# Kernel tuning notes

Measured on AMD Instinct MI355X. Metric: run time of the kernel, lower is better.

The kernel has to match this reference:

```python
import jax, jax.numpy as jnp
import numpy as np

NS = 100000  # senders
NR = 100000  # receivers
E = 600000   # edges
D = 128      # sender_dim = receiver_dim = edge_dim
EPS = 1e-5


def _layer_norm(x, g, b):
    mu = jnp.mean(x, axis=-1, keepdims=True)
    var = jnp.mean(jnp.square(x - mu), axis=-1, keepdims=True)
    return (x - mu) * jax.lax.rsqrt(var + EPS) * g + b


def _gcast_mlp(x, W, b, gamma, beta):
    # Faithful to GCastMLP.forward: z = silu(linear(x)); z = LN(silu(z))
    z = jax.nn.silu(x @ W.T + b)
    return _layer_norm(jax.nn.silu(z), gamma, beta)


def setup_inputs() -> dict:
    key = jax.random.key(0)
    ks = jax.random.split(key, 12)
    s = 1.0 / np.sqrt(3 * D)
    inp = {
        "sender_x": jax.random.normal(ks[0], (NS, D), jnp.float32),
        "receiver_x": jax.random.normal(ks[1], (NR, D), jnp.float32),
        "edge_index": jax.random.randint(ks[2], (2, E), 0, NR, jnp.int32),
        "edge_attr": jax.random.normal(ks[3], (E, D), jnp.float32),
        # edge MLP: in = sender+receiver+edge = 3D, out = edge_dim
        "We": jax.random.uniform(ks[4], (D, 3 * D), jnp.float32, -s, s),
        "be": jnp.zeros((D,), jnp.float32),
        "ge": jnp.ones((D,), jnp.float32),
        "bbe": jnp.zeros((D,), jnp.float32),
        # node MLP: in = receiver+edge = 2D, out = receiver_dim
        "Wn": jax.random.uniform(ks[5], (D, 2 * D), jnp.float32, -1.0 / np.sqrt(2 * D), 1.0 / np.sqrt(2 * D)),
        "bn": jnp.zeros((D,), jnp.float32),
        "gn": jnp.ones((D,), jnp.float32),
        "bbn": jnp.zeros((D,), jnp.float32),
        # sender MLP: square D -> D
        "Ws": jax.random.uniform(ks[6], (D, D), jnp.float32, -1.0 / np.sqrt(D), 1.0 / np.sqrt(D)),
        "bs": jnp.zeros((D,), jnp.float32),
        "gs": jnp.ones((D,), jnp.float32),
        "bbs": jnp.zeros((D,), jnp.float32),
    }
    return inp


def reference(sender_x, receiver_x, edge_index, edge_attr,
              We, be, ge, bbe, Wn, bn, gn, bbn, Ws, bs, gs, bbs):
    src, dst = edge_index[0], edge_index[1]
    # Edge encoder: gather endpoints, concat, MLP -> new edge features [E, D]
    edge_in = jnp.concatenate([sender_x[src], receiver_x[dst], edge_attr], axis=-1)
    edge_attr_p = _gcast_mlp(edge_in, We, be, ge, bbe)
    # Node encoder: scatter-sum messages (= new edge features) to receivers
    edge_aggr = jax.ops.segment_sum(edge_attr_p, dst, num_segments=receiver_x.shape[0])
    mesh_x_p = _gcast_mlp(jnp.concatenate([receiver_x, edge_aggr], axis=-1), Wn, bn, gn, bbn)
    # Residual updates
    sender_out = sender_x + _gcast_mlp(sender_x, Ws, bs, gs, bbs)
    receiver_out = receiver_x + mesh_x_p
    edge_out = edge_attr + edge_attr_p
    return (sender_out, receiver_out, edge_out)
```

## Files before the change

kernel.cpp:

```cpp
#include <hip/hip_runtime.h>
#include <stdint.h>


typedef __bf16 bf16x8 __attribute__((ext_vector_type(8)));
typedef float  f32x4  __attribute__((ext_vector_type(4)));

union U16B { uint4 u; bf16x8 v; };
union BFPK { __bf16 h[2]; unsigned int u; };
union BF1  { __bf16 h; unsigned short s; };

__device__ __forceinline__ float silu_f(float x) {
  return x * __builtin_amdgcn_rcpf(1.0f + __expf(-x));
}
__device__ __forceinline__ float bfu2f(unsigned int lo16) {
  return __uint_as_float(lo16 << 16);
}
__device__ __forceinline__ bf16x8 cvt8(float4 a, float4 b) {
  bf16x8 r;
  r[0] = (__bf16)a.x; r[1] = (__bf16)a.y; r[2] = (__bf16)a.z; r[3] = (__bf16)a.w;
  r[4] = (__bf16)b.x; r[5] = (__bf16)b.y; r[6] = (__bf16)b.z; r[7] = (__bf16)b.w;
  return r;
}

__global__ void cvt_weights_kernel(const float* __restrict__ We,
                                   const float* __restrict__ Wn,
                                   const float* __restrict__ Ws,
                                   unsigned short* __restrict__ out) {
  int i = blockIdx.x * 256 + threadIdx.x;
  if (i >= 6 * 16384) return;
  int panel = i >> 14;
  int r = (i >> 7) & 127;
  int csw = i & 127;
  int c_or = ((csw * 2) ^ ((r & 7) << 4)) >> 1;
  float f;
  if (panel < 3)      f = We[r * 384 + panel * 128 + c_or];
  else if (panel < 5) f = Wn[r * 256 + (panel - 3) * 128 + c_or];
  else                f = Ws[r * 128 + c_or];
  BF1 c; c.h = (__bf16)f;
  out[i] = c.s;
}

__global__ void cvt_rows_kernel(const float* __restrict__ in,
                                unsigned short* __restrict__ out, int n8) {
  int i = blockIdx.x * 256 + threadIdx.x;
  if (i >= n8) return;
  float4 a = reinterpret_cast<const float4*>(in)[2 * i];
  float4 b = reinterpret_cast<const float4*>(in)[2 * i + 1];
  U16B r; r.v = cvt8(a, b);
  reinterpret_cast<uint4*>(out)[i] = r.u;
}

__global__ void hist_kernel(const int* __restrict__ dst, int* __restrict__ counts, int E) {
  int i = blockIdx.x * 256 + threadIdx.x;
  if (i < E) atomicAdd(&counts[dst[i]], 1);
}

__global__ void scan1_kernel(const int* __restrict__ counts, int* __restrict__ pre,
                             int* __restrict__ blockSums, int n) {
  __shared__ int sh[256];
  const int t = threadIdx.x;
  const int base = blockIdx.x * 1024 + t * 4;
  int c0 = (base + 0 < n) ? counts[base + 0] : 0;
  int c1 = (base + 1 < n) ? counts[base + 1] : 0;
  int c2 = (base + 2 < n) ? counts[base + 2] : 0;
  int c3 = (base + 3 < n) ? counts[base + 3] : 0;
  int tot = c0 + c1 + c2 + c3;
  sh[t] = tot;
  __syncthreads();
  #pragma unroll
  for (int off = 1; off < 256; off <<= 1) {
    int v = (t >= off) ? sh[t - off] : 0;
    __syncthreads();
    sh[t] += v;
    __syncthreads();
  }
  int excl = sh[t] - tot;
  if (base + 0 < n) pre[base + 0] = excl;
  if (base + 1 < n) pre[base + 1] = excl + c0;
  if (base + 2 < n) pre[base + 2] = excl + c0 + c1;
  if (base + 3 < n) pre[base + 3] = excl + c0 + c1 + c2;
  if (t == 255) blockSums[blockIdx.x] = sh[255];
}

__global__ void scan2_kernel(int* __restrict__ blockSums, int nb) {
  __shared__ int sh[512];
  const int t = threadIdx.x;
  int v = (t < nb) ? blockSums[t] : 0;
  sh[t] = v;
  __syncthreads();
  #pragma unroll
  for (int off = 1; off < 512; off <<= 1) {
    int u = (t >= off) ? sh[t - off] : 0;
    __syncthreads();
    sh[t] += u;
    __syncthreads();
  }
  if (t < nb) blockSums[t] = sh[t] - v;
}

__global__ void scan3_kernel(const int* __restrict__ pre, const int* __restrict__ blockSums,
                             int* __restrict__ offs, int* __restrict__ cursor, int n) {
  int i = blockIdx.x * 256 + threadIdx.x;
  if (i >= n) return;
  int o = pre[i] + blockSums[i >> 10];
  offs[i] = o;
  cursor[i] = o;
}

__global__ void scatter_kernel(const int* __restrict__ dst, int* __restrict__ cursor,
                               int* __restrict__ rank, int E) {
  int i = blockIdx.x * 256 + threadIdx.x;
  if (i < E) {
    int p = atomicAdd(&cursor[dst[i]], 1);
    rank[i] = p;
  }
}

__global__ __launch_bounds__(256) void agg_kernel(
    const unsigned short* __restrict__ P,
    const int* __restrict__ offs, const int* __restrict__ counts,
    unsigned short* __restrict__ aggr, int NR) {
  const int l = threadIdx.x & 31;
  const int g0 = (blockIdx.x * 256 + threadIdx.x) >> 5;
  if (g0 >= NR) return;
  int beg = offs[g0];
  int cnt = counts[g0];
  float s0 = 0.f, s1 = 0.f, s2 = 0.f, s3 = 0.f;
  const unsigned short* p = P + (size_t)beg * 128 + l * 4;
  for (int k = 0; k < cnt; ++k) {
    uint2 w = *reinterpret_cast<const uint2*>(p);
    p += 128;
    s0 += bfu2f(w.x & 0xffffu);
    s1 += bfu2f(w.x >> 16);
    s2 += bfu2f(w.y & 0xffffu);
    s3 += bfu2f(w.y >> 16);
  }
  BFPK a, b;
  a.h[0] = (__bf16)s0; a.h[1] = (__bf16)s1;
  b.h[0] = (__bf16)s2; b.h[1] = (__bf16)s3;
  uint2 o; o.x = a.u; o.y = b.u;
  *reinterpret_cast<uint2*>(aggr + (size_t)g0 * 128 + l * 4) = o;
}

template <int KDIM, int AGGR, bool S0B, bool S1B>
__global__ __launch_bounds__(512, 4) void mlp_v8_kernel(
    const void* __restrict__ s0v, const int* __restrict__ i0,
    const void* __restrict__ s1v, const int* __restrict__ i1,
    const float* __restrict__ s2,
    const unsigned short* __restrict__ Wb,
    const float* __restrict__ bias, const float* __restrict__ gamma,
    const float* __restrict__ beta,
    const float* __restrict__ resid,
    float* __restrict__ outp,
    void* aggr, const int* __restrict__ aggr_idx,
    const int* __restrict__ prank,
    int M) {
  constexpr int NSEG = KDIM / 128;
  __shared__ __align__(16) unsigned short smem[2][16384];

  const int tid = threadIdx.x;
  const int wid = tid >> 6;
  const int lane = tid & 63;
  const int l15 = lane & 15;
  const int q = lane >> 4;
  const int l31 = lane & 31;
  const int rhalf = lane >> 5;
  const int wrow = blockIdx.x * 128 + wid * 16;
  const int xm = (l15 & 7) << 3;

  int rr = wrow + l15;
  if (rr >= M) rr = M - 1;
  const unsigned short* p0b; const float* p0f;
  const unsigned short* p1b = nullptr; const float* p1f = nullptr;
  const float* p2 = nullptr;
  {
    int r0 = i0 ? i0[rr] : rr;
    if constexpr (S0B) p0b = (const unsigned short*)s0v + (size_t)r0 * 128;
    else               p0f = (const float*)s0v + (size_t)r0 * 128;
    if constexpr (KDIM >= 256) {
      int r1 = i1 ? i1[rr] : rr;
      if constexpr (S1B) p1b = (const unsigned short*)s1v + (size_t)r1 * 128;
      else               p1f = (const float*)s1v + (size_t)r1 * 128;
    }
    if constexpr (KDIM >= 384) p2 = s2 + (size_t)rr * 128;
  }

  f32x4 acc[8] = {};

  auto stageB = [&](int seg, int buf) {
    const unsigned short* g = Wb + seg * 16384 + wid * 2048 + lane * 8;
    unsigned short* l = &smem[buf][wid * 2048];
    #pragma unroll
    for (int u = 0; u < 4; ++u) {
      __builtin_amdgcn_global_load_lds(
          (const __attribute__((address_space(1))) unsigned int*)(g + u * 512),
          (__attribute__((address_space(3))) unsigned int*)(l + u * 512),
          16, 0, 0);
    }
  };

  U16B Ac[4], An[4];
  auto loadA = [&](int seg, U16B (&dst)[4]) {
    #pragma unroll
    for (int k4 = 0; k4 < 4; ++k4) {
      const int kof = k4 * 32 + q * 8;
      if (seg == 0) {
        if constexpr (S0B) {
          dst[k4].u = *reinterpret_cast<const uint4*>(p0b + kof);
        } else {
          const float4* p = reinterpret_cast<const float4*>(p0f + kof);
          dst[k4].v = cvt8(p[0], p[1]);
        }
      } else if (seg == 1) {
        if constexpr (S1B) {
          dst[k4].u = *reinterpret_cast<const uint4*>(p1b + kof);
        } else {
          const float4* p = reinterpret_cast<const float4*>(p1f + kof);
          dst[k4].v = cvt8(p[0], p[1]);
        }
      } else {
        const float4* p = reinterpret_cast<const float4*>(p2 + kof);
        dst[k4].v = cvt8(p[0], p[1]);
      }
    }
  };

  stageB(0, 0);
  loadA(0, Ac);
  __syncthreads();

  int cur = 0;
  #pragma unroll
  for (int seg = 0; seg < NSEG; ++seg) {
    if (seg + 1 < NSEG) {
      stageB(seg + 1, cur ^ 1);
      loadA(seg + 1, An);
    }
    #pragma unroll
    for (int k4 = 0; k4 < 4; ++k4) {
      #pragma unroll
      for (int n = 0; n < 8; ++n) {
        U16B b;
        b.u = *reinterpret_cast<const uint4*>(
            &smem[cur][(n * 16 + l15) * 128 + ((k4 * 32 + q * 8) ^ xm)]);
        acc[n] = __builtin_amdgcn_mfma_f32_16x16x32_bf16(Ac[k4].v, b.v, acc[n], 0, 0, 0);
      }
    }
    __syncthreads();
    if (seg + 1 < NSEG) {
      #pragma unroll
      for (int k4 = 0; k4 < 4; ++k4) Ac[k4] = An[k4];
      cur ^= 1;
    }
  }

  float bia[8];
  #pragma unroll
  for (int n = 0; n < 8; ++n) bia[n] = bias[n * 16 + l15];

  float sum[4] = {0.f, 0.f, 0.f, 0.f};
  float ssq[4] = {0.f, 0.f, 0.f, 0.f};
  #pragma unroll
  for (int n = 0; n < 8; ++n) {
    #pragma unroll
    for (int j = 0; j < 4; ++j) {
      float t = silu_f(silu_f(acc[n][j] + bia[n]));
      acc[n][j] = t;
      sum[j] += t;
      ssq[j] += t * t;
    }
  }
  #pragma unroll
  for (int off = 1; off < 16; off <<= 1) {
    #pragma unroll
    for (int j = 0; j < 4; ++j) {
      sum[j] += __shfl_xor(sum[j], off);
      ssq[j] += __shfl_xor(ssq[j], off);
    }
  }
  float mu[4], rs[4];
  #pragma unroll
  for (int j = 0; j < 4; ++j) {
    mu[j] = sum[j] * (1.0f / 128.0f);
    float var = ssq[j] * (1.0f / 128.0f) - mu[j] * mu[j];
    rs[j] = rsqrtf(var + 1e-5f);
  }
  float gam[8], bet[8];
  #pragma unroll
  for (int n = 0; n < 8; ++n) {
    gam[n] = gamma[n * 16 + l15];
    bet[n] = beta[n * 16 + l15];
  }

  unsigned short* yw = &smem[0][0] + wid * (16 * 132);
  #pragma unroll
  for (int n = 0; n < 8; ++n) {
    #pragma unroll
    for (int j = 0; j < 4; ++j) {
      float y = (acc[n][j] - mu[j]) * rs[j] * gam[n] + bet[n];
      BF1 c; c.h = (__bf16)y;
      yw[(q * 4 + j) * 132 + n * 16 + l15] = c.s;
    }
  }
  asm volatile("s_waitcnt lgkmcnt(0)" ::: "memory");

  #pragma unroll
  for (int s = 0; s < 8; ++s) {
    int row16 = 2 * s + rhalf;
    int grow = wrow + row16;
    uint2 w = *reinterpret_cast<const uint2*>(&yw[row16 * 132 + l31 * 4]);
    if (grow < M) {
      const f32x4 r4 = *reinterpret_cast<const f32x4*>(resid + (size_t)grow * 128 + l31 * 4);
      f32x4 o4;
      o4.x = r4.x + bfu2f(w.x & 0xffffu);
      o4.y = r4.y + bfu2f(w.x >> 16);
      o4.z = r4.z + bfu2f(w.y & 0xffffu);
      o4.w = r4.w + bfu2f(w.y >> 16);
      __builtin_nontemporal_store(o4, reinterpret_cast<f32x4*>(outp + (size_t)grow * 128 + l31 * 4));
      if constexpr (AGGR == 3) {
        int prow = prank[grow];
        *reinterpret_cast<uint2*>((unsigned short*)aggr + (size_t)prow * 128 + l31 * 4) = w;
      } else if constexpr (AGGR == 2) {
        int idx = aggr_idx[grow];
        unsigned short* ar = (unsigned short*)aggr + (size_t)idx * 128 + l31 * 4;
        asm volatile("global_atomic_pk_add_bf16 %0, %1, off" :: "v"(ar), "v"(w.x) : "memory");
        asm volatile("global_atomic_pk_add_bf16 %0, %1, off" :: "v"(ar + 2), "v"(w.y) : "memory");
      } else if constexpr (AGGR == 1) {
        int idx = aggr_idx[grow];
        float* ar = (float*)aggr + (size_t)idx * 128 + l31 * 4;
        atomicAdd(ar + 0, bfu2f(w.x & 0xffffu));
        atomicAdd(ar + 1, bfu2f(w.x >> 16));
        atomicAdd(ar + 2, bfu2f(w.y & 0xffffu));
        atomicAdd(ar + 3, bfu2f(w.y >> 16));
      }
    }
  }
}

extern "C" void kernel_launch(void* const* d_in, const int* in_sizes, int n_in,
                              void* d_out, int out_size, void* d_ws, size_t ws_size,
                              hipStream_t stream) {
  const float* sender_x   = (const float*)d_in[0];
  const float* receiver_x = (const float*)d_in[1];
  const int*   edge_index = (const int*)d_in[2];
  const float* edge_attr  = (const float*)d_in[3];
  const float* We  = (const float*)d_in[4];
  const float* be  = (const float*)d_in[5];
  const float* ge  = (const float*)d_in[6];
  const float* bbe = (const float*)d_in[7];
  const float* Wn  = (const float*)d_in[8];
  const float* bn  = (const float*)d_in[9];
  const float* gn  = (const float*)d_in[10];
  const float* bbn = (const float*)d_in[11];
  const float* Ws  = (const float*)d_in[12];
  const float* bs  = (const float*)d_in[13];
  const float* gs  = (const float*)d_in[14];
  const float* bbs = (const float*)d_in[15];

  const int D  = 128;
  const int NS = in_sizes[0] / D;
  const int NR = in_sizes[1] / D;
  const int E  = in_sizes[2] / 2;

  const int* src = edge_index;
  const int* dst = edge_index + E;

  float* out          = (float*)d_out;
  float* sender_out   = out;
  float* receiver_out = out + (size_t)NS * D;
  float* edge_out     = out + (size_t)(NS + NR) * D;

  const size_t welems = 6 * 16384;
  unsigned short* We_b = (unsigned short*)d_ws;
  unsigned short* Wn_b = We_b + 3 * 16384;
  unsigned short* Ws_b = We_b + 5 * 16384;
  unsigned short* sender_b   = We_b + welems;
  unsigned short* receiver_b = sender_b + (size_t)NS * D;
  unsigned short* aggr_b     = receiver_b + (size_t)NR * D;
  unsigned short* P_b        = aggr_b + (size_t)NR * D;
  int* counts    = (int*)(P_b + (size_t)E * D);
  int* pre       = counts + NR;
  int* offs      = pre + NR;
  int* cursor    = offs + NR;
  int* blockSums = cursor + NR;
  int* rank      = blockSums + 512;

  const int nScanBlocks = (NR + 1023) / 1024;
  const size_t needCSR = 2 * (welems + (size_t)(NS + 2 * NR) * D + (size_t)E * D)
                       + 4 * (4 * (size_t)NR + 512 + (size_t)E);
  const size_t needA = (welems + (size_t)(NS + 2 * NR) * D) * 2;
  const size_t needB = (welems + (size_t)NR * D) * 2;
  unsigned short* aggrB = We_b + welems;

  int tier;
  if (ws_size >= needCSR && nScanBlocks <= 512) tier = 0;
  else if (ws_size >= needA) tier = 1;
  else if (ws_size >= needB) tier = 2;
  else tier = 3;

  cvt_weights_kernel<<<(int)((welems + 255) / 256), 256, 0, stream>>>(We, Wn, Ws, We_b);

  const int gridE = (E + 127) / 128;
  const int gridR = (NR + 127) / 128;
  const int gridS = (NS + 127) / 128;
  const int n8s = NS * D / 8, n8r = NR * D / 8;

  if (tier == 0) {
    cvt_rows_kernel<<<(n8s + 255) / 256, 256, 0, stream>>>(sender_x, sender_b, n8s);
    cvt_rows_kernel<<<(n8r + 255) / 256, 256, 0, stream>>>(receiver_x, receiver_b, n8r);

    (void)hipMemsetAsync(counts, 0, (size_t)NR * 4, stream);
    hist_kernel<<<(E + 255) / 256, 256, 0, stream>>>(dst, counts, E);
    scan1_kernel<<<nScanBlocks, 256, 0, stream>>>(counts, pre, blockSums, NR);
    scan2_kernel<<<1, 512, 0, stream>>>(blockSums, nScanBlocks);
    scan3_kernel<<<(NR + 255) / 256, 256, 0, stream>>>(pre, blockSums, offs, cursor, NR);
    scatter_kernel<<<(E + 255) / 256, 256, 0, stream>>>(dst, cursor, rank, E);

    mlp_v8_kernel<384, 3, true, true><<<gridE, 512, 0, stream>>>(
        sender_b, src, receiver_b, dst, edge_attr,
        We_b, be, ge, bbe, edge_attr, edge_out, P_b, nullptr, rank, E);

    agg_kernel<<<(NR + 7) / 8, 256, 0, stream>>>(P_b, offs, counts, aggr_b, NR);

    mlp_v8_kernel<256, 0, true, true><<<gridR, 512, 0, stream>>>(
        receiver_b, nullptr, aggr_b, nullptr, nullptr,
        Wn_b, bn, gn, bbn, receiver_x, receiver_out, nullptr, nullptr, nullptr, NR);

    mlp_v8_kernel<128, 0, true, false><<<gridS, 512, 0, stream>>>(
        sender_b, nullptr, nullptr, nullptr, nullptr,
        Ws_b, bs, gs, bbs, sender_x, sender_out, nullptr, nullptr, nullptr, NS);
  } else if (tier == 1) {
    cvt_rows_kernel<<<(n8s + 255) / 256, 256, 0, stream>>>(sender_x, sender_b, n8s);
    cvt_rows_kernel<<<(n8r + 255) / 256, 256, 0, stream>>>(receiver_x, receiver_b, n8r);
    (void)hipMemsetAsync(aggr_b, 0, (size_t)NR * D * 2, stream);

    mlp_v8_kernel<384, 2, true, true><<<gridE, 512, 0, stream>>>(
        sender_b, src, receiver_b, dst, edge_attr,
        We_b, be, ge, bbe, edge_attr, edge_out, aggr_b, dst, nullptr, E);

    mlp_v8_kernel<256, 0, true, true><<<gridR, 512, 0, stream>>>(
        receiver_b, nullptr, aggr_b, nullptr, nullptr,
        Wn_b, bn, gn, bbn, receiver_x, receiver_out, nullptr, nullptr, nullptr, NR);

    mlp_v8_kernel<128, 0, true, false><<<gridS, 512, 0, stream>>>(
        sender_b, nullptr, nullptr, nullptr, nullptr,
        Ws_b, bs, gs, bbs, sender_x, sender_out, nullptr, nullptr, nullptr, NS);
  } else if (tier == 2) {
    (void)hipMemsetAsync(aggrB, 0, (size_t)NR * D * 2, stream);

    mlp_v8_kernel<384, 2, false, false><<<gridE, 512, 0, stream>>>(
        sender_x, src, receiver_x, dst, edge_attr,
        We_b, be, ge, bbe, edge_attr, edge_out, aggrB, dst, nullptr, E);

    mlp_v8_kernel<256, 0, false, true><<<gridR, 512, 0, stream>>>(
        receiver_x, nullptr, aggrB, nullptr, nullptr,
        Wn_b, bn, gn, bbn, receiver_x, receiver_out, nullptr, nullptr, nullptr, NR);

    mlp_v8_kernel<128, 0, false, false><<<gridS, 512, 0, stream>>>(
        sender_x, nullptr, nullptr, nullptr, nullptr,
        Ws_b, bs, gs, bbs, sender_x, sender_out, nullptr, nullptr, nullptr, NS);
  } else {
    (void)hipMemsetAsync(receiver_out, 0, (size_t)NR * D * sizeof(float), stream);

    mlp_v8_kernel<384, 1, false, false><<<gridE, 512, 0, stream>>>(
        sender_x, src, receiver_x, dst, edge_attr,
        We_b, be, ge, bbe, edge_attr, edge_out, receiver_out, dst, nullptr, E);

    mlp_v8_kernel<256, 0, false, false><<<gridR, 512, 0, stream>>>(
        receiver_x, nullptr, receiver_out, nullptr, nullptr,
        Wn_b, bn, gn, bbn, receiver_x, receiver_out, nullptr, nullptr, nullptr, NR);

    mlp_v8_kernel<128, 0, false, false><<<gridS, 512, 0, stream>>>(
        sender_x, nullptr, nullptr, nullptr, nullptr,
        Ws_b, bs, gs, bbs, sender_x, sender_out, nullptr, nullptr, nullptr, NS);
  }
}
```

Measured before the change: 461.6 us.

## Prefetch all A operands and weight panels upfront, widen LDS swizzle, fuse prep kernels

The MLP kernel now issues every A-operand global load (all segments) and the first two weight panels at the start, before any MFMA runs. This replaces the per-segment double-buffered prefetch and exposes more memory-level parallelism. The LDS XOR swizzle widens from 8 to 16 rows to cut bank conflicts on B reads. The weight conversion and the two row-conversion kernels merge into one prep launch, and the fp32 fallback tiers move to a separate simpler kernel. Holding all A operands in registers at once raises register pressure, which may hurt occupancy under the 512x4 launch bounds.

```diff
diff --git a/kernel.cpp b/kernel.cpp
--- a/kernel.cpp
+++ b/kernel.cpp
@@ -22,32 +22,38 @@
   return r;
 }
 
-__global__ void cvt_weights_kernel(const float* __restrict__ We,
-                                   const float* __restrict__ Wn,
-                                   const float* __restrict__ Ws,
-                                   unsigned short* __restrict__ out) {
+__global__ void prep_kernel(const float* __restrict__ We,
+                            const float* __restrict__ Wn,
+                            const float* __restrict__ Ws,
+                            unsigned short* __restrict__ wimg,
+                            const float* __restrict__ sx,
+                            unsigned short* __restrict__ sb,
+                            const float* __restrict__ rx,
+                            unsigned short* __restrict__ rb,
+                            int n8s, int n8r) {
   int i = blockIdx.x * 256 + threadIdx.x;
-  if (i >= 6 * 16384) return;
-  int panel = i >> 14;
-  int r = (i >> 7) & 127;
-  int csw = i & 127;
-  int c_or = ((csw * 2) ^ ((r & 7) << 4)) >> 1;
-  float f;
-  if (panel < 3)      f = We[r * 384 + panel * 128 + c_or];
-  else if (panel < 5) f = Wn[r * 256 + (panel - 3) * 128 + c_or];
-  else                f = Ws[r * 128 + c_or];
-  BF1 c; c.h = (__bf16)f;
-  out[i] = c.s;
-}
-
-__global__ void cvt_rows_kernel(const float* __restrict__ in,
-                                unsigned short* __restrict__ out, int n8) {
-  int i = blockIdx.x * 256 + threadIdx.x;
-  if (i >= n8) return;
-  float4 a = reinterpret_cast<const float4*>(in)[2 * i];
-  float4 b = reinterpret_cast<const float4*>(in)[2 * i + 1];
-  U16B r; r.v = cvt8(a, b);
-  reinterpret_cast<uint4*>(out)[i] = r.u;
+  if (i < 6 * 16384) {
+    int panel = i >> 14;
+    int r = (i >> 7) & 127;
+    int csw = i & 127;
+    int c_or = ((csw * 2) ^ ((r & 15) << 4)) >> 1;
+    float f;
+    if (panel < 3)      f = We[r * 384 + panel * 128 + c_or];
+    else if (panel < 5) f = Wn[r * 256 + (panel - 3) * 128 + c_or];
+    else                f = Ws[r * 128 + c_or];
+    BF1 c; c.h = (__bf16)f;
+    wimg[i] = c.s;
+    return;
+  }
+  int j = i - 6 * 16384;
+  const float* in; unsigned short* out; int idx;
+  if (j < n8s) { in = sx; out = sb; idx = j; }
+  else if (j < n8s + n8r) { in = rx; out = rb; idx = j - n8s; }
+  else return;
+  float4 a = reinterpret_cast<const float4*>(in)[2 * idx];
+  float4 b = reinterpret_cast<const float4*>(in)[2 * idx + 1];
+  U16B r8; r8.v = cvt8(a, b);
+  reinterpret_cast<uint4*>(out)[idx] = r8.u;
 }
 
 __global__ void hist_kernel(const int* __restrict__ dst, int* __restrict__ counts, int E) {
@@ -142,10 +148,10 @@
   *reinterpret_cast<uint2*>(aggr + (size_t)g0 * 128 + l * 4) = o;
 }
 
-template <int KDIM, int AGGR, bool S0B, bool S1B>
-__global__ __launch_bounds__(512, 4) void mlp_v8_kernel(
-    const void* __restrict__ s0v, const int* __restrict__ i0,
-    const void* __restrict__ s1v, const int* __restrict__ i1,
+template <int KDIM, int AGGR>
+__global__ __launch_bounds__(512, 4) void mlp_v9_kernel(
+    const unsigned short* __restrict__ s0, const int* __restrict__ i0,
+    const unsigned short* __restrict__ s1, const int* __restrict__ i1,
     const float* __restrict__ s2,
     const unsigned short* __restrict__ Wb,
     const float* __restrict__ bias, const float* __restrict__ gamma,
@@ -166,26 +172,15 @@
   const int l31 = lane & 31;
   const int rhalf = lane >> 5;
   const int wrow = blockIdx.x * 128 + wid * 16;
-  const int xm = (l15 & 7) << 3;
+  const int xm = l15 << 3;
 
   int rr = wrow + l15;
   if (rr >= M) rr = M - 1;
-  const unsigned short* p0b; const float* p0f;
-  const unsigned short* p1b = nullptr; const float* p1f = nullptr;
+  const unsigned short* p0 = s0 + (size_t)(i0 ? i0[rr] : rr) * 128;
+  const unsigned short* p1 = nullptr;
   const float* p2 = nullptr;
-  {
-    int r0 = i0 ? i0[rr] : rr;
-    if constexpr (S0B) p0b = (const unsigned short*)s0v + (size_t)r0 * 128;
-    else               p0f = (const float*)s0v + (size_t)r0 * 128;
-    if constexpr (KDIM >= 256) {
-      int r1 = i1 ? i1[rr] : rr;
-      if constexpr (S1B) p1b = (const unsigned short*)s1v + (size_t)r1 * 128;
-      else               p1f = (const float*)s1v + (size_t)r1 * 128;
-    }
-    if constexpr (KDIM >= 384) p2 = s2 + (size_t)rr * 128;
-  }
-
-  f32x4 acc[8] = {};
+  if constexpr (KDIM >= 256) p1 = s1 + (size_t)(i1 ? i1[rr] : rr) * 128;
+  if constexpr (KDIM >= 384) p2 = s2 + (size_t)rr * 128;
 
   auto stageB = [&](int seg, int buf) {
     const unsigned short* g = Wb + seg * 16384 + wid * 2048 + lane * 8;
@@ -199,60 +194,54 @@
     }
   };
 
-  U16B Ac[4], An[4];
-  auto loadA = [&](int seg, U16B (&dst)[4]) {
-    #pragma unroll
-    for (int k4 = 0; k4 < 4; ++k4) {
-      const int kof = k4 * 32 + q * 8;
-      if (seg == 0) {
-        if constexpr (S0B) {
-          dst[k4].u = *reinterpret_cast<const uint4*>(p0b + kof);
-        } else {
-          const float4* p = reinterpret_cast<const float4*>(p0f + kof);
-          dst[k4].v = cvt8(p[0], p[1]);
-        }
-      } else if (seg == 1) {
-        if constexpr (S1B) {
-          dst[k4].u = *reinterpret_cast<const uint4*>(p1b + kof);
-        } else {
-          const float4* p = reinterpret_cast<const float4*>(p1f + kof);
-          dst[k4].v = cvt8(p[0], p[1]);
-        }
-      } else {
-        const float4* p = reinterpret_cast<const float4*>(p2 + kof);
-        dst[k4].v = cvt8(p[0], p[1]);
-      }
-    }
-  };
-
   stageB(0, 0);
-  loadA(0, Ac);
+  if constexpr (NSEG > 1) stageB(1, 1);
+
+  U16B A0[4], A1[4];
+  float4 A2r[8];
+  #pragma unroll
+  for (int k4 = 0; k4 < 4; ++k4) {
+    A0[k4].u = *reinterpret_cast<const uint4*>(p0 + k4 * 32 + q * 8);
+    if constexpr (KDIM >= 256)
+      A1[k4].u = *reinterpret_cast<const uint4*>(p1 + k4 * 32 + q * 8);
+    if constexpr (KDIM >= 384) {
+      A2r[2 * k4]     = reinterpret_cast<const float4*>(p2 + k4 * 32 + q * 8)[0];
+      A2r[2 * k4 + 1] = reinterpret_cast<const float4*>(p2 + k4 * 32 + q * 8)[1];
+    }
+  }
+  __builtin_amdgcn_sched_barrier(0);
   __syncthreads();
 
-  int cur = 0;
-  #pragma unroll
-  for (int seg = 0; seg < NSEG; ++seg) {
-    if (seg + 1 < NSEG) {
-      stageB(seg + 1, cur ^ 1);
-      loadA(seg + 1, An);
-    }
+  f32x4 acc[8] = {};
+
+  auto mfmaSeg = [&](int buf, const U16B (&A)[4]) {
     #pragma unroll
     for (int k4 = 0; k4 < 4; ++k4) {
       #pragma unroll
       for (int n = 0; n < 8; ++n) {
         U16B b;
         b.u = *reinterpret_cast<const uint4*>(
-            &smem[cur][(n * 16 + l15) * 128 + ((k4 * 32 + q * 8) ^ xm)]);
-        acc[n] = __builtin_amdgcn_mfma_f32_16x16x32_bf16(Ac[k4].v, b.v, acc[n], 0, 0, 0);
+            &smem[buf][(n * 16 + l15) * 128 + ((k4 * 32 + q * 8) ^ xm)]);
+        acc[n] = __builtin_amdgcn_mfma_f32_16x16x32_bf16(A[k4].v, b.v, acc[n], 0, 0, 0);
       }
     }
+  };
+
+  mfmaSeg(0, A0);
+  if constexpr (NSEG >= 2) {
     __syncthreads();
-    if (seg + 1 < NSEG) {
+    if constexpr (NSEG >= 3) stageB(2, 0);
+    mfmaSeg(1, A1);
+    if constexpr (NSEG >= 3) {
+      __syncthreads();
+      U16B A2[4];
       #pragma unroll
-      for (int k4 = 0; k4 < 4; ++k4) Ac[k4] = An[k4];
-      cur ^= 1;
-    }
-  }
+      for (int k4 = 0; k4 < 4; ++k4) A2[k4].v = cvt8(A2r[2 * k4], A2r[2 * k4 + 1]);
+      mfmaSeg(0, A2);
+    }
+  }
+
+  unsigned short* yw = (NSEG == 2 ? &smem[0][0] : &smem[1][0]) + wid * (16 * 132);
 
   float bia[8];
   #pragma unroll
@@ -292,7 +281,6 @@
     bet[n] = beta[n * 16 + l15];
   }
 
-  unsigned short* yw = &smem[0][0] + wid * (16 * 132);
   #pragma unroll
   for (int n = 0; n < 8; ++n) {
     #pragma unroll
@@ -325,9 +313,131 @@
         unsigned short* ar = (unsigned short*)aggr + (size_t)idx * 128 + l31 * 4;
         asm volatile("global_atomic_pk_add_bf16 %0, %1, off" :: "v"(ar), "v"(w.x) : "memory");
         asm volatile("global_atomic_pk_add_bf16 %0, %1, off" :: "v"(ar + 2), "v"(w.y) : "memory");
-      } else if constexpr (AGGR == 1) {
+      }
+    }
+  }
+}
+
+template <int KDIM>
+__global__ __launch_bounds__(512, 4) void mlp_fb_kernel(
+    const float* __restrict__ s0, const int* __restrict__ i0,
+    const float* __restrict__ s1, const int* __restrict__ i1,
+    const float* __restrict__ s2,
+    const unsigned short* __restrict__ Wb,
+    const float* __restrict__ bias, const float* __restrict__ gamma,
+    const float* __restrict__ beta,
+    const float* __restrict__ resid,
+    float* __restrict__ outp,
+    float* aggr, const int* __restrict__ aggr_idx,
+    int M) {
+  constexpr int NSEG = KDIM / 128;
+  __shared__ __align__(16) unsigned short smem[2][16384];
+  const int tid = threadIdx.x;
+  const int wid = tid >> 6;
+  const int lane = tid & 63;
+  const int l15 = lane & 15;
+  const int q = lane >> 4;
+  const int l31 = lane & 31;
+  const int rhalf = lane >> 5;
+  const int wrow = blockIdx.x * 128 + wid * 16;
+  const int xm = l15 << 3;
+
+  int rr = wrow + l15;
+  if (rr >= M) rr = M - 1;
+  const float* p0 = s0 + (size_t)(i0 ? i0[rr] : rr) * 128;
+  const float* p1 = (KDIM >= 256) ? (s1 + (size_t)(i1 ? i1[rr] : rr) * 128) : nullptr;
+  const float* p2 = (KDIM >= 384) ? (s2 + (size_t)rr * 128) : nullptr;
+
+  auto stageB = [&](int seg, int buf) {
+    const unsigned short* g = Wb + seg * 16384 + wid * 2048 + lane * 8;
+    unsigned short* l = &smem[buf][wid * 2048];
+    #pragma unroll
+    for (int u = 0; u < 4; ++u) {
+      __builtin_amdgcn_global_load_lds(
+          (const __attribute__((address_space(1))) unsigned int*)(g + u * 512),
+          (__attribute__((address_space(3))) unsigned int*)(l + u * 512),
+          16, 0, 0);
+    }
+  };
+
+  stageB(0, 0);
+  f32x4 acc[8] = {};
+  __syncthreads();
+  int cur = 0;
+  #pragma unroll
+  for (int seg = 0; seg < NSEG; ++seg) {
+    if (seg + 1 < NSEG) stageB(seg + 1, cur ^ 1);
+    const float* base = (seg == 0) ? p0 : ((seg == 1) ? p1 : p2);
+    #pragma unroll
+    for (int k4 = 0; k4 < 4; ++k4) {
+      const float4* pp = reinterpret_cast<const float4*>(base + k4 * 32 + q * 8);
+      U16B a; a.v = cvt8(pp[0], pp[1]);
+      #pragma unroll
+      for (int n = 0; n < 8; ++n) {
+        U16B b;
+        b.u = *reinterpret_cast<const uint4*>(
+            &smem[cur][(n * 16 + l15) * 128 + ((k4 * 32 + q * 8) ^ xm)]);
+        acc[n] = __builtin_amdgcn_mfma_f32_16x16x32_bf16(a.v, b.v, acc[n], 0, 0, 0);
+      }
+    }
+    __syncthreads();
+    if (seg + 1 < NSEG) cur ^= 1;
+  }
+
+  unsigned short* yw = &smem[0][0] + wid * (16 * 132);
+  float bia[8];
+  #pragma unroll
+  for (int n = 0; n < 8; ++n) bia[n] = bias[n * 16 + l15];
+  float sum[4] = {0.f, 0.f, 0.f, 0.f}, ssq[4] = {0.f, 0.f, 0.f, 0.f};
+  #pragma unroll
+  for (int n = 0; n < 8; ++n)
+    #pragma unroll
+    for (int j = 0; j < 4; ++j) {
+      float t = silu_f(silu_f(acc[n][j] + bia[n]));
+      acc[n][j] = t; sum[j] += t; ssq[j] += t * t;
+    }
+  #pragma unroll
+  for (int off = 1; off < 16; off <<= 1)
+    #pragma unroll
+    for (int j = 0; j < 4; ++j) {
+      sum[j] += __shfl_xor(sum[j], off);
+      ssq[j] += __shfl_xor(ssq[j], off);
+    }
+  float mu[4], rs[4];
+  #pragma unroll
+  for (int j = 0; j < 4; ++j) {
+    mu[j] = sum[j] * (1.0f / 128.0f);
+    float var = ssq[j] * (1.0f / 128.0f) - mu[j] * mu[j];
+    rs[j] = rsqrtf(var + 1e-5f);
+  }
+  float gam[8], bet[8];
+  #pragma unroll
+  for (int n = 0; n < 8; ++n) { gam[n] = gamma[n * 16 + l15]; bet[n] = beta[n * 16 + l15]; }
+  #pragma unroll
+  for (int n = 0; n < 8; ++n)
+    #pragma unroll
+    for (int j = 0; j < 4; ++j) {
+      float y = (acc[n][j] - mu[j]) * rs[j] * gam[n] + bet[n];
+      BF1 c; c.h = (__bf16)y;
+      yw[(q * 4 + j) * 132 + n * 16 + l15] = c.s;
+    }
+  asm volatile("s_waitcnt lgkmcnt(0)" ::: "memory");
+  #pragma unroll
+  for (int s = 0; s < 8; ++s) {
+    int row16 = 2 * s + rhalf;
+    int grow = wrow + row16;
+    uint2 w = *reinterpret_cast<const uint2*>(&yw[row16 * 132 + l31 * 4]);
+    if (grow < M) {
+      const f32x4 r4 = *reinterpret_cast<const f32x4*>(resid + (size_t)grow * 128 + l31 * 4);
+      f32x4 o4;
+      o4.x = r4.x + bfu2f(w.x & 0xffffu);
+      o4.y = r4.y + bfu2f(w.x >> 16);
+      o4.z = r4.z + bfu2f(w.y & 0xffffu);
+      o4.w = r4.w + bfu2f(w.y >> 16);
+      __builtin_nontemporal_store(o4, reinterpret_cast<f32x4*>(outp + (size_t)grow * 128 + l31 * 4));
+      if (aggr) {
         int idx = aggr_idx[grow];
-        float* ar = (float*)aggr + (size_t)idx * 128 + l31 * 4;
+        float* ar = aggr + (size_t)idx * 128 + l31 * 4;
         atomicAdd(ar + 0, bfu2f(w.x & 0xffffu));
         atomicAdd(ar + 1, bfu2f(w.x >> 16));
         atomicAdd(ar + 2, bfu2f(w.y & 0xffffu));
@@ -389,26 +499,27 @@
   const size_t needCSR = 2 * (welems + (size_t)(NS + 2 * NR) * D + (size_t)E * D)
                        + 4 * (4 * (size_t)NR + 512 + (size_t)E);
   const size_t needA = (welems + (size_t)(NS + 2 * NR) * D) * 2;
-  const size_t needB = (welems + (size_t)NR * D) * 2;
-  unsigned short* aggrB = We_b + welems;
 
   int tier;
   if (ws_size >= needCSR && nScanBlocks <= 512) tier = 0;
   else if (ws_size >= needA) tier = 1;
-  else if (ws_size >= needB) tier = 2;
-  else tier = 3;
-
-  cvt_weights_kernel<<<(int)((welems + 255) / 256), 256, 0, stream>>>(We, Wn, Ws, We_b);
+  else tier = 2;
 
   const int gridE = (E + 127) / 128;
   const int gridR = (NR + 127) / 128;
   const int gridS = (NS + 127) / 128;
   const int n8s = NS * D / 8, n8r = NR * D / 8;
 
+  if (tier <= 1) {
+    const int prepItems = (int)welems + n8s + n8r;
+    prep_kernel<<<(prepItems + 255) / 256, 256, 0, stream>>>(
+        We, Wn, Ws, We_b, sender_x, sender_b, receiver_x, receiver_b, n8s, n8r);
+  } else {
+    prep_kernel<<<(int)((welems + 255) / 256), 256, 0, stream>>>(
+        We, Wn, Ws, We_b, nullptr, nullptr, nullptr, nullptr, 0, 0);
+  }
+
   if (tier == 0) {
-    cvt_rows_kernel<<<(n8s + 255) / 256, 256, 0, stream>>>(sender_x, sender_b, n8s);
-    cvt_rows_kernel<<<(n8r + 255) / 256, 256, 0, stream>>>(receiver_x, receiver_b, n8r);
-
     (void)hipMemsetAsync(counts, 0, (size_t)NR * 4, stream);
     hist_kernel<<<(E + 255) / 256, 256, 0, stream>>>(dst, counts, E);
     scan1_kernel<<<nScanBlocks, 256, 0, stream>>>(counts, pre, blockSums, NR);
@@ -416,62 +527,46 @@
     scan3_kernel<<<(NR + 255) / 256, 256, 0, stream>>>(pre, blockSums, offs, cursor, NR);
     scatter_kernel<<<(E + 255) / 256, 256, 0, stream>>>(dst, cursor, rank, E);
 
-    mlp_v8_kernel<384, 3, true, true><<<gridE, 512, 0, stream>>>(
+    mlp_v9_kernel<384, 3><<<gridE, 512, 0, stream>>>(
         sender_b, src, receiver_b, dst, edge_attr,
         We_b, be, ge, bbe, edge_attr, edge_out, P_b, nullptr, rank, E);
 
     agg_kernel<<<(NR + 7) / 8, 256, 0, stream>>>(P_b, offs, counts, aggr_b, NR);
 
-    mlp_v8_kernel<256, 0, true, true><<<gridR, 512, 0, stream>>>(
+    mlp_v9_kernel<256, 0><<<gridR, 512, 0, stream>>>(
         receiver_b, nullptr, aggr_b, nullptr, nullptr,
         Wn_b, bn, gn, bbn, receiver_x, receiver_out, nullptr, nullptr, nullptr, NR);
 
-    mlp_v8_kernel<128, 0, true, false><<<gridS, 512, 0, stream>>>(
+    mlp_v9_kernel<128, 0><<<gridS, 512, 0, stream>>>(
         sender_b, nullptr, nullptr, nullptr, nullptr,
         Ws_b, bs, gs, bbs, sender_x, sender_out, nullptr, nullptr, nullptr, NS);
   } else if (tier == 1) {
-    cvt_rows_kernel<<<(n8s + 255) / 256, 256, 0, stream>>>(sender_x, sender_b, n8s);
-    cvt_rows_kernel<<<(n8r + 255) / 256, 256, 0, stream>>>(receiver_x, receiver_b, n8r);
     (void)hipMemsetAsync(aggr_b, 0, (size_t)NR * D * 2, stream);
 
-    mlp_v8_kernel<384, 2, true, true><<<gridE, 512, 0, stream>>>(
+    mlp_v9_kernel<384, 2><<<gridE, 512, 0, stream>>>(
         sender_b, src, receiver_b, dst, edge_attr,
         We_b, be, ge, bbe, edge_attr, edge_out, aggr_b, dst, nullptr, E);
 
-    mlp_v8_kernel<256, 0, true, true><<<gridR, 512, 0, stream>>>(
+    mlp_v9_kernel<256, 0><<<gridR, 512, 0, stream>>>(
         receiver_b, nullptr, aggr_b, nullptr, nullptr,
         Wn_b, bn, gn, bbn, receiver_x, receiver_out, nullptr, nullptr, nullptr, NR);
 
-    mlp_v8_kernel<128, 0, true, false><<<gridS, 512, 0, stream>>>(
+    mlp_v9_kernel<128, 0><<<gridS, 512, 0, stream>>>(
         sender_b, nullptr, nullptr, nullptr, nullptr,
-        Ws_b, bs, gs, bbs, sender_x, sender_out, nullptr, nullptr, nullptr, NS);
-  } else if (tier == 2) {
-    (void)hipMemsetAsync(aggrB, 0, (size_t)NR * D * 2, stream);
-
-    mlp_v8_kernel<384, 2, false, false><<<gridE, 512, 0, stream>>>(
-        sender_x, src, receiver_x, dst, edge_attr,
-        We_b, be, ge, bbe, edge_attr, edge_out, aggrB, dst, nullptr, E);
-
-    mlp_v8_kernel<256, 0, false, true><<<gridR, 512, 0, stream>>>(
-        receiver_x, nullptr, aggrB, nullptr, nullptr,
-        Wn_b, bn, gn, bbn, receiver_x, receiver_out, nullptr, nullptr, nullptr, NR);
-
-    mlp_v8_kernel<128, 0, false, false><<<gridS, 512, 0, stream>>>(
-        sender_x, nullptr, nullptr, nullptr, nullptr,
         Ws_b, bs, gs, bbs, sender_x, sender_out, nullptr, nullptr, nullptr, NS);
   } else {
     (void)hipMemsetAsync(receiver_out, 0, (size_t)NR * D * sizeof(float), stream);
 
-    mlp_v8_kernel<384, 1, false, false><<<gridE, 512, 0, stream>>>(
+    mlp_fb_kernel<384><<<gridE, 512, 0, stream>>>(
         sender_x, src, receiver_x, dst, edge_attr,
-        We_b, be, ge, bbe, edge_attr, edge_out, receiver_out, dst, nullptr, E);
-
-    mlp_v8_kernel<256, 0, false, false><<<gridR, 512, 0, stream>>>(
+        We_b, be, ge, bbe, edge_attr, edge_out, receiver_out, dst, E);
+
+    mlp_fb_kernel<256><<<gridR, 512, 0, stream>>>(
         receiver_x, nullptr, receiver_out, nullptr, nullptr,
-        Wn_b, bn, gn, bbn, receiver_x, receiver_out, nullptr, nullptr, nullptr, NR);
-
-    mlp_v8_kernel<128, 0, false, false><<<gridS, 512, 0, stream>>>(
+        Wn_b, bn, gn, bbn, receiver_x, receiver_out, nullptr, nullptr, NR);
+
+    mlp_fb_kernel<128><<<gridS, 512, 0, stream>>>(
         sender_x, nullptr, nullptr, nullptr, nullptr,
-        Ws_b, bs, gs, bbs, sender_x, sender_out, nullptr, nullptr, nullptr, NS);
-  }
-}
+        Ws_b, bs, gs, bbs, sender_x, sender_out, nullptr, nullptr, NS);
+  }
+}
```

Result: no change. 454.5 us (-1.5%).
